# Performance work log

Measured on AMD Instinct MI355X. Metric: run time of the kernel, lower is better.

Reference implementation:

```python
import jax, jax.numpy as jnp
import numpy as np

N_NODES, N_EDGES, HIDDEN, N_LAYERS, VOCAB = 50000, 800000, 64, 2, 100

def silu(v):
    return v * jax.nn.sigmoid(v)

def setup_inputs() -> dict:
    key = jax.random.key(0)
    ks = jax.random.split(key, 18)
    N, E, H, L = N_NODES, N_EDGES, HIDDEN, N_LAYERS
    atomic_numbers = jax.random.randint(ks[0], (N,), 0, VOCAB)
    pos = jax.random.normal(ks[1], (N, 3), jnp.float32)
    edge_index = jax.random.randint(ks[2], (2, E), 0, N)
    edge_attr = jax.random.normal(ks[3], (E, 4), jnp.float32)
    emb = (jax.random.normal(ks[4], (VOCAB, H), jnp.float32) * 0.1).at[0].set(0.0)  # padding_idx=0
    def w(k, shape):
        return jax.random.normal(k, shape, jnp.float32) * (1.0 / np.sqrt(shape[-2]))
    return {
        'atomic_numbers': atomic_numbers, 'pos': pos,
        'edge_index': edge_index, 'edge_attr': edge_attr, 'emb': emb,
        # phi_e: Linear(2H+1,H) -> SiLU -> Linear(H,H) -> SiLU, stacked over layers
        'e_w1': w(ks[5], (L, 2 * H + 1, H)), 'e_b1': jnp.zeros((L, H), jnp.float32),
        'e_w2': w(ks[6], (L, H, H)),         'e_b2': jnp.zeros((L, H), jnp.float32),
        # phi_h: Linear(2H,H) -> SiLU -> Linear(H,H)
        'h_w1': w(ks[7], (L, 2 * H, H)),     'h_b1': jnp.zeros((L, H), jnp.float32),
        'h_w2': w(ks[8], (L, H, H)),         'h_b2': jnp.zeros((L, H), jnp.float32),
        # phi_x: Linear(H,H) -> SiLU -> Linear(H,1)
        'x_w1': w(ks[9], (L, H, H)),         'x_b1': jnp.zeros((L, H), jnp.float32),
        'x_w2': w(ks[10], (L, H, 1)),        'x_b2': jnp.zeros((L, 1), jnp.float32),
    }

def reference(atomic_numbers, pos, edge_index, edge_attr, emb,
              e_w1, e_b1, e_w2, e_b2, h_w1, h_b1, h_w2, h_b2,
              x_w1, x_b1, x_w2, x_b2):
    N = pos.shape[0]
    src, dst = edge_index[0], edge_index[1]  # PyG: h_j = h[src], h_i = h[dst]; aggregate to dst
    h = emb[atomic_numbers]  # [N, H]
    x = pos
    for l in range(N_LAYERS):
        x_diff = x[src] - x[dst]                       # [E, 3]
        r_ij = jnp.linalg.norm(x_diff, axis=-1, keepdims=True)  # [E, 1]
        feat = jnp.concatenate([h[dst], h[src], r_ij], axis=-1)  # [E, 2H+1]
        m_ij = silu(silu(feat @ e_w1[l] + e_b1[l]) @ e_w2[l] + e_b2[l])  # [E, H]
        W_ij = silu(m_ij @ x_w1[l] + x_b1[l]) @ x_w2[l] + x_b2[l]        # [E, 1]
        x = x + jax.ops.segment_sum(W_ij * x_diff, dst, num_segments=N)
        m_i = jax.ops.segment_sum(m_ij, dst, num_segments=N)             # [N, H]
        hm = jnp.concatenate([h, m_i], axis=-1)                          # [N, 2H]
        h = h + (silu(hm @ h_w1[l] + h_b1[l]) @ h_w2[l] + h_b2[l])
    return h, x
```

## Files before the change

### kernel.cpp

```cpp
#include <hip/hip_runtime.h>

#define NN 50000
#define NE 800000
#define HD 64
#define NL 2
#define NT_E (NE / 16)
#define NT_N (NN / 16)
#define NCH 196

typedef __attribute__((ext_vector_type(4))) float f32x4;
typedef __attribute__((ext_vector_type(8))) short s16x8;

#define FLAG_OFF 0
#define WB_OFF   16
#define EMB_O 0
#define EW1_O 6400
#define EB1_O 22912
#define EW2_O 23040
#define EB2_O 31232
#define HW1_O 31360
#define HB1_O 47744
#define HW2_O 47872
#define HB2_O 56064
#define XW1_O 56192
#define XB1_O 64384
#define XW2_O 64512
#define XB2_O 64640
#define X_OFF    (WB_OFF + 64656)
#define MAGG_OFF (X_OFF + NN * 4)
#define XAGG_OFF (MAGG_OFF + NN * HD)
#define HBF_OFF  (XAGG_OFF + NN * 3)
#define CNT_OFF  (HBF_OFF + NN * 32)
#define CSUM_OFF (CNT_OFF + NCH * 256)
#define INCL_OFF (CSUM_OFF + 256)
#define PAIR_OFF (INCL_OFF + NCH * 256)

#define ROWP 72

__device__ __forceinline__ float bf2f(unsigned short u) {
    return __uint_as_float(((unsigned int)u) << 16);
}
__device__ __forceinline__ unsigned short f2bf(float f) {
    unsigned int i = __float_as_uint(f);
    i += 0x7fffu + ((i >> 16) & 1u);
    return (unsigned short)(i >> 16);
}
__device__ __forceinline__ unsigned short f2bf_t(float f) {
    return (unsigned short)(__float_as_uint(f) >> 16);
}
__device__ __forceinline__ float silu(float v) {
    const float e = __expf(-v);
    return v * __builtin_amdgcn_rcpf(1.0f + e);
}
__device__ __forceinline__ float ldf(const void* p, int i, int bf) {
    return bf ? bf2f(((const unsigned short*)p)[i]) : ((const float*)p)[i];
}

__global__ void detect_kernel(const unsigned short* __restrict__ pos, int* __restrict__ flag) {
    const int lane = threadIdx.x;
    const float v = bf2f(pos[2 * lane]);
    const float a = fabsf(v);
    const int ok = (a >= 1e-6f && a <= 1e6f) ? 1 : 0;
    const unsigned long long m = __ballot(ok);
    if (lane == 0) *flag = (__popcll(m) >= 32) ? 1 : 0;
}

__global__ __launch_bounds__(256) void convert_kernel(
    const void* pos, const void* emb,
    const void* ew1, const void* eb1, const void* ew2, const void* eb2,
    const void* hw1, const void* hb1, const void* hw2, const void* hb2,
    const void* xw1, const void* xb1, const void* xw2, const void* xb2,
    float* __restrict__ wbuf, float* __restrict__ x, const int* __restrict__ flag)
{
    const int bf = *flag;
    const int tid = blockIdx.x * blockDim.x + threadIdx.x;
    const int stride = gridDim.x * blockDim.x;
    for (int n = tid; n < NN; n += stride) {
        x[n * 4 + 0] = ldf(pos, n * 3 + 0, bf);
        x[n * 4 + 1] = ldf(pos, n * 3 + 1, bf);
        x[n * 4 + 2] = ldf(pos, n * 3 + 2, bf);
        x[n * 4 + 3] = 0.f;
    }
    for (int i = tid; i < 6400; i += stride) wbuf[EMB_O + i] = ldf(emb, i, bf);
    for (int i = tid; i < 16512; i += stride) wbuf[EW1_O + i] = ldf(ew1, i, bf);
    for (int i = tid; i < 128; i += stride) wbuf[EB1_O + i] = ldf(eb1, i, bf);
    for (int i = tid; i < 8192; i += stride) wbuf[EW2_O + i] = ldf(ew2, i, bf);
    for (int i = tid; i < 128; i += stride) wbuf[EB2_O + i] = ldf(eb2, i, bf);
    for (int i = tid; i < 16384; i += stride) wbuf[HW1_O + i] = ldf(hw1, i, bf);
    for (int i = tid; i < 128; i += stride) wbuf[HB1_O + i] = ldf(hb1, i, bf);
    for (int i = tid; i < 8192; i += stride) wbuf[HW2_O + i] = ldf(hw2, i, bf);
    for (int i = tid; i < 128; i += stride) wbuf[HB2_O + i] = ldf(hb2, i, bf);
    for (int i = tid; i < 8192; i += stride) wbuf[XW1_O + i] = ldf(xw1, i, bf);
    for (int i = tid; i < 128; i += stride) wbuf[XB1_O + i] = ldf(xb1, i, bf);
    for (int i = tid; i < 128; i += stride) wbuf[XW2_O + i] = ldf(xw2, i, bf);
    for (int i = tid; i < 2; i += stride) wbuf[XB2_O + i] = ldf(xb2, i, bf);
}

__global__ __launch_bounds__(256) void init_h_kernel(
    const int* __restrict__ an, const float* __restrict__ embf,
    unsigned short* __restrict__ h_bf)
{
    const int stride = gridDim.x * blockDim.x;
    for (int i = blockIdx.x * blockDim.x + threadIdx.x; i < NN * HD; i += stride) {
        int a = an[i >> 6];
        a = (a < 0) ? 0 : (a > 99 ? 99 : a);
        h_bf[i] = f2bf(embf[a * HD + (i & 63)]);
    }
}

__global__ __launch_bounds__(256) void hist_kernel(const int* __restrict__ ei, int* __restrict__ cnt) {
    const int stride = gridDim.x * blockDim.x;
    for (int e = blockIdx.x * blockDim.x + threadIdx.x; e < NE; e += stride) {
        int d = ei[NE + e];
        d = (d < 0) ? 0 : (d >= NN ? NN - 1 : d);
        atomicAdd(&cnt[d], 1);
    }
}

__global__ __launch_bounds__(256) void scan1_kernel(
    const int* __restrict__ cnt, int* __restrict__ incl, int* __restrict__ csum)
{
    __shared__ int s[256];
    const int t = threadIdx.x, b = blockIdx.x, i = b * 256 + t;
    s[t] = cnt[i];
    __syncthreads();
#pragma unroll
    for (int o = 1; o < 256; o <<= 1) {
        const int u = (t >= o) ? s[t - o] : 0;
        __syncthreads();
        s[t] += u;
        __syncthreads();
    }
    incl[i] = s[t];
    if (t == 255) csum[b] = s[255];
}

__global__ void scan2_kernel(int* __restrict__ csum) {
    __shared__ int s[256];
    const int t = threadIdx.x;
    s[t] = (t < NCH) ? csum[t] : 0;
    __syncthreads();
#pragma unroll
    for (int o = 1; o < 256; o <<= 1) {
        const int u = (t >= o) ? s[t - o] : 0;
        __syncthreads();
        s[t] += u;
        __syncthreads();
    }
    if (t < NCH) csum[t] = s[t];
}

__global__ __launch_bounds__(256) void scan3_kernel(
    int* __restrict__ cnt, const int* __restrict__ incl, const int* __restrict__ csum)
{
    const int t = threadIdx.x, b = blockIdx.x, i = b * 256 + t;
    const int off = (b > 0) ? csum[b - 1] : 0;
    cnt[i] = incl[i] - cnt[i] + off;
}

__global__ __launch_bounds__(256) void scatter_kernel(
    const int* __restrict__ ei, int* __restrict__ cur, int2* __restrict__ pair)
{
    const int stride = gridDim.x * blockDim.x;
    for (int e = blockIdx.x * blockDim.x + threadIdx.x; e < NE; e += stride) {
        int s = ei[e];
        int d = ei[NE + e];
        s = (s < 0) ? 0 : (s >= NN ? NN - 1 : s);
        d = (d < 0) ? 0 : (d >= NN ? NN - 1 : d);
        const int p = atomicAdd(&cur[d], 1);
        pair[p] = make_int2(s, d);
    }
}

__global__ __launch_bounds__(256, 4) void edge_mfma_kernel(
    const unsigned short* __restrict__ h_bf, const float* __restrict__ x,
    const int2* __restrict__ pair,
    const float* __restrict__ w1, const float* __restrict__ b1,
    const float* __restrict__ b2,
    const float* __restrict__ w2,
    const float* __restrict__ xw1, const float* __restrict__ xb1,
    const float* __restrict__ xw2, const float* __restrict__ xb2,
    float* __restrict__ m_agg, float* __restrict__ x_agg)
{
    __shared__ unsigned short s_w1p[4 * 4 * 64 * 8];
    __shared__ unsigned short s_xw1p[2 * 4 * 64 * 8];
    __shared__ unsigned short s_act[4][16 * ROWP];
    __shared__ float s_xd[4][16][4];
    __shared__ float s_wv[4][16];

    const int tid = threadIdx.x;
    for (int p = tid; p < 4 * 4 * 64 * 8; p += 256) {
        const int j = p & 7, ln = (p >> 3) & 63, nt = (p >> 9) & 3, kc = p >> 11;
        const int k = kc * 32 + (ln >> 4) * 8 + j, n = nt * 16 + (ln & 15);
        s_w1p[p] = f2bf(w1[k * 64 + n]);
    }
    for (int p = tid; p < 2 * 4 * 64 * 8; p += 256) {
        const int j = p & 7, ln = (p >> 3) & 63, nt = (p >> 9) & 3, kc = p >> 11;
        const int k = kc * 32 + (ln >> 4) * 8 + j, n = nt * 16 + (ln & 15);
        s_xw1p[p] = f2bf(xw1[k * 64 + n]);
    }
    __syncthreads();

    const int lane = tid & 63;
    const int wid = tid >> 6;
    const int l15 = lane & 15;
    const int q = lane >> 4;

    s16x8 bw2[2][4];
#pragma unroll
    for (int kc = 0; kc < 2; ++kc)
#pragma unroll
        for (int nt = 0; nt < 4; ++nt)
#pragma unroll
            for (int j = 0; j < 8; ++j)
                bw2[kc][nt][j] = (short)f2bf(w2[(kc * 32 + q * 8 + j) * 64 + nt * 16 + l15]);

    float b1v[4], b2v[4], xb1v[4], xw2v[4], wrv[4];
#pragma unroll
    for (int nt = 0; nt < 4; ++nt) {
        b1v[nt] = b1[nt * 16 + l15];
        b2v[nt] = b2[nt * 16 + l15];
        xb1v[nt] = xb1[nt * 16 + l15];
        xw2v[nt] = xw2[nt * 16 + l15];
        wrv[nt] = w1[128 * 64 + nt * 16 + l15];
    }
    const float xb2v = xb2[0];

    unsigned short* act = s_act[wid];
    float (*xd)[4] = s_xd[wid];
    float* wv = s_wv[wid];

    const int gwave = (blockIdx.x << 2) + wid;
    const int nwaves = gridDim.x << 2;

    for (int t = gwave; t < NT_E; t += nwaves) {
        const int e0 = t * 16;
        const int2 e = pair[e0 + l15];
        const int sidx = e.x, didx = e.y;
        const f32x4 xs = *(const f32x4*)&x[sidx * 4];
        const f32x4 xdv = *(const f32x4*)&x[didx * 4];
        const float ax = xs[0] - xdv[0];
        const float ay = xs[1] - xdv[1];
        const float az = xs[2] - xdv[2];
        const float rme = sqrtf(ax * ax + ay * ay + az * az);
        if (lane < 16) { xd[lane][0] = ax; xd[lane][1] = ay; xd[lane][2] = az; }

        const s16x8 a_hd0 = *(const s16x8*)&h_bf[didx * 64 + q * 8];
        const s16x8 a_hd1 = *(const s16x8*)&h_bf[didx * 64 + 32 + q * 8];
        const s16x8 a_hs0 = *(const s16x8*)&h_bf[sidx * 64 + q * 8];
        const s16x8 a_hs1 = *(const s16x8*)&h_bf[sidx * 64 + 32 + q * 8];

        f32x4 acc[4];
#pragma unroll
        for (int nt = 0; nt < 4; ++nt) acc[nt] = (f32x4){0.f, 0.f, 0.f, 0.f};
#pragma unroll
        for (int kc = 0; kc < 4; ++kc) {
            const s16x8 a = (kc == 0) ? a_hd0 : (kc == 1) ? a_hd1 : (kc == 2) ? a_hs0 : a_hs1;
#pragma unroll
            for (int nt = 0; nt < 4; ++nt) {
                const s16x8 b = *(const s16x8*)&s_w1p[((kc * 4 + nt) * 64 + lane) * 8];
                acc[nt] = __builtin_amdgcn_mfma_f32_16x16x32_bf16(a, b, acc[nt], 0, 0, 0);
            }
        }
        float rv[4];
#pragma unroll
        for (int r = 0; r < 4; ++r) rv[r] = __shfl(rme, q * 4 + r, 64);
#pragma unroll
        for (int nt = 0; nt < 4; ++nt)
#pragma unroll
            for (int r = 0; r < 4; ++r) {
                const float v = silu(acc[nt][r] + b1v[nt] + rv[r] * wrv[nt]);
                act[(q * 4 + r) * ROWP + nt * 16 + l15] = f2bf_t(v);
            }

        f32x4 acc2[4];
#pragma unroll
        for (int nt = 0; nt < 4; ++nt) acc2[nt] = (f32x4){0.f, 0.f, 0.f, 0.f};
#pragma unroll
        for (int kc = 0; kc < 2; ++kc) {
            const s16x8 a = *(const s16x8*)&act[l15 * ROWP + kc * 32 + q * 8];
#pragma unroll
            for (int nt = 0; nt < 4; ++nt)
                acc2[nt] = __builtin_amdgcn_mfma_f32_16x16x32_bf16(a, bw2[kc][nt], acc2[nt], 0, 0, 0);
        }
#pragma unroll
        for (int nt = 0; nt < 4; ++nt)
#pragma unroll
            for (int r = 0; r < 4; ++r) {
                const float v = silu(acc2[nt][r] + b2v[nt]);
                act[(q * 4 + r) * ROWP + nt * 16 + l15] = f2bf_t(v);
            }

        f32x4 xacc[4];
#pragma unroll
        for (int nt = 0; nt < 4; ++nt) xacc[nt] = (f32x4){0.f, 0.f, 0.f, 0.f};
#pragma unroll
        for (int kc = 0; kc < 2; ++kc) {
            const s16x8 a = *(const s16x8*)&act[l15 * ROWP + kc * 32 + q * 8];
#pragma unroll
            for (int nt = 0; nt < 4; ++nt) {
                const s16x8 b = *(const s16x8*)&s_xw1p[((kc * 4 + nt) * 64 + lane) * 8];
                xacc[nt] = __builtin_amdgcn_mfma_f32_16x16x32_bf16(a, b, xacc[nt], 0, 0, 0);
            }
        }
        float ssum[4];
#pragma unroll
        for (int r = 0; r < 4; ++r) {
            float s = 0.f;
#pragma unroll
            for (int nt = 0; nt < 4; ++nt)
                s += silu(xacc[nt][r] + xb1v[nt]) * xw2v[nt];
            ssum[r] = s;
        }
#pragma unroll
        for (int off = 1; off < 16; off <<= 1)
#pragma unroll
            for (int r = 0; r < 4; ++r) ssum[r] += __shfl_xor(ssum[r], off, 64);
        if (l15 == 0) {
#pragma unroll
            for (int r = 0; r < 4; ++r) wv[q * 4 + r] = ssum[r] + xb2v;
        }

        int dstv[17];
#pragma unroll
        for (int rr = 0; rr < 16; ++rr) dstv[rr] = __shfl(didx, rr, 64);
        dstv[16] = -1;

        float macc = 0.f;
#pragma unroll
        for (int rr = 0; rr < 16; ++rr) {
            macc += bf2f(act[rr * ROWP + lane]);
            if (dstv[rr + 1] != dstv[rr]) {
                atomicAdd(&m_agg[dstv[rr] * 64 + lane], macc);
                macc = 0.f;
            }
        }
        if (lane < 3) {
            float xac = 0.f;
#pragma unroll
            for (int rr = 0; rr < 16; ++rr) {
                xac += wv[rr] * xd[rr][lane];
                if (dstv[rr + 1] != dstv[rr]) {
                    atomicAdd(&x_agg[dstv[rr] * 3 + lane], xac);
                    xac = 0.f;
                }
            }
        }
    }
}

__global__ __launch_bounds__(256, 4) void node_mfma_kernel(
    float* __restrict__ x,
    const float* __restrict__ m_agg, const float* __restrict__ x_agg,
    const float* __restrict__ w1, const float* __restrict__ b1,
    const float* __restrict__ w2, const float* __restrict__ b2,
    unsigned short* __restrict__ h_bf,
    void* __restrict__ outv, const int* __restrict__ flag)
{
    __shared__ unsigned short s_w1p[4 * 4 * 64 * 8];
    __shared__ unsigned short s_act[4][16 * ROWP];

    const int tid = threadIdx.x;
    for (int p = tid; p < 4 * 4 * 64 * 8; p += 256) {
        const int j = p & 7, ln = (p >> 3) & 63, nt = (p >> 9) & 3, kc = p >> 11;
        const int k = kc * 32 + (ln >> 4) * 8 + j, n = nt * 16 + (ln & 15);
        s_w1p[p] = f2bf(w1[k * 64 + n]);
    }
    __syncthreads();

    const int bf = flag ? *flag : 1;
    const int lane = tid & 63;
    const int wid = tid >> 6;
    const int l15 = lane & 15;
    const int q = lane >> 4;

    for (int n = blockIdx.x * 256 + tid; n < NN; n += gridDim.x * 256) {
#pragma unroll
        for (int c = 0; c < 3; ++c) {
            const float xn = x[n * 4 + c] + x_agg[n * 3 + c];
            x[n * 4 + c] = xn;
            if (outv) {
                if (bf) ((unsigned short*)outv)[NN * HD + n * 3 + c] = f2bf(xn);
                else ((float*)outv)[NN * HD + n * 3 + c] = xn;
            }
        }
    }

    s16x8 bw2[2][4];
#pragma unroll
    for (int kc = 0; kc < 2; ++kc)
#pragma unroll
        for (int nt = 0; nt < 4; ++nt)
#pragma unroll
            for (int j = 0; j < 8; ++j)
                bw2[kc][nt][j] = (short)f2bf(w2[(kc * 32 + q * 8 + j) * 64 + nt * 16 + l15]);

    float b1v[4], b2v[4];
#pragma unroll
    for (int nt = 0; nt < 4; ++nt) {
        b1v[nt] = b1[nt * 16 + l15];
        b2v[nt] = b2[nt * 16 + l15];
    }
    unsigned short* act = s_act[wid];

    for (int t = (blockIdx.x << 2) + wid; t < NT_N; t += gridDim.x << 2) {
        const int n = t * 16 + l15;
        const s16x8 a0 = *(const s16x8*)&h_bf[n * 64 + q * 8];
        const s16x8 a1 = *(const s16x8*)&h_bf[n * 64 + 32 + q * 8];
        const f32x4 m0 = *(const f32x4*)&m_agg[n * 64 + q * 8];
        const f32x4 m1 = *(const f32x4*)&m_agg[n * 64 + q * 8 + 4];
        const f32x4 m2 = *(const f32x4*)&m_agg[n * 64 + 32 + q * 8];
        const f32x4 m3 = *(const f32x4*)&m_agg[n * 64 + 32 + q * 8 + 4];
        s16x8 a2, a3;
#pragma unroll
        for (int j = 0; j < 4; ++j) {
            a2[j] = (short)f2bf(m0[j]); a2[4 + j] = (short)f2bf(m1[j]);
            a3[j] = (short)f2bf(m2[j]); a3[4 + j] = (short)f2bf(m3[j]);
        }

        f32x4 acc[4];
#pragma unroll
        for (int nt = 0; nt < 4; ++nt) acc[nt] = (f32x4){0.f, 0.f, 0.f, 0.f};
#pragma unroll
        for (int kc = 0; kc < 4; ++kc) {
            const s16x8 a = (kc == 0) ? a0 : (kc == 1) ? a1 : (kc == 2) ? a2 : a3;
#pragma unroll
            for (int nt = 0; nt < 4; ++nt) {
                const s16x8 b = *(const s16x8*)&s_w1p[((kc * 4 + nt) * 64 + lane) * 8];
                acc[nt] = __builtin_amdgcn_mfma_f32_16x16x32_bf16(a, b, acc[nt], 0, 0, 0);
            }
        }
#pragma unroll
        for (int nt = 0; nt < 4; ++nt)
#pragma unroll
            for (int r = 0; r < 4; ++r)
                act[(q * 4 + r) * ROWP + nt * 16 + l15] = f2bf_t(silu(acc[nt][r] + b1v[nt]));

        f32x4 acc2[4];
#pragma unroll
        for (int nt = 0; nt < 4; ++nt) acc2[nt] = (f32x4){0.f, 0.f, 0.f, 0.f};
#pragma unroll
        for (int kc = 0; kc < 2; ++kc) {
            const s16x8 a = *(const s16x8*)&act[l15 * ROWP + kc * 32 + q * 8];
#pragma unroll
            for (int nt = 0; nt < 4; ++nt)
                acc2[nt] = __builtin_amdgcn_mfma_f32_16x16x32_bf16(a, bw2[kc][nt], acc2[nt], 0, 0, 0);
        }
#pragma unroll
        for (int nt = 0; nt < 4; ++nt)
#pragma unroll
            for (int r = 0; r < 4; ++r) {
                const int row = t * 16 + q * 4 + r, col = nt * 16 + l15;
                const float hn = bf2f(h_bf[row * 64 + col]) + acc2[nt][r] + b2v[nt];
                h_bf[row * 64 + col] = f2bf(hn);
                if (outv) {
                    if (bf) ((unsigned short*)outv)[row * 64 + col] = f2bf(hn);
                    else ((float*)outv)[row * 64 + col] = hn;
                }
            }
    }
}

extern "C" void kernel_launch(void* const* d_in, const int* in_sizes, int n_in,
                              void* d_out, int out_size, void* d_ws, size_t ws_size,
                              hipStream_t stream) {
    const int* an = (const int*)d_in[0];
    const void* pos = d_in[1];
    const int* ei = (const int*)d_in[2];

    int wi = 4;
    if (n_in > 4 && in_sizes[4] == 6400) wi = 4;
    else if (n_in > 3 && in_sizes[3] == 6400) wi = 3;
    const void* emb = d_in[wi];
    const void* e_w1 = d_in[wi + 1];
    const void* e_b1 = d_in[wi + 2];
    const void* e_w2 = d_in[wi + 3];
    const void* e_b2 = d_in[wi + 4];
    const void* h_w1 = d_in[wi + 5];
    const void* h_b1 = d_in[wi + 6];
    const void* h_w2 = d_in[wi + 7];
    const void* h_b2 = d_in[wi + 8];
    const void* x_w1 = d_in[wi + 9];
    const void* x_b1 = d_in[wi + 10];
    const void* x_w2 = d_in[wi + 11];
    const void* x_b2 = d_in[wi + 12];

    float* ws = (float*)d_ws;
    int* flag = (int*)(ws + FLAG_OFF);
    float* wbuf = ws + WB_OFF;
    float* x = ws + X_OFF;
    float* m_agg = ws + MAGG_OFF;
    float* x_agg = ws + XAGG_OFF;
    unsigned short* h_bf = (unsigned short*)(ws + HBF_OFF);
    int* cnt = (int*)(ws + CNT_OFF);
    int* csum = (int*)(ws + CSUM_OFF);
    int* incl = (int*)(ws + INCL_OFF);
    int2* pair = (int2*)(ws + PAIR_OFF);

    detect_kernel<<<1, 64, 0, stream>>>((const unsigned short*)pos, flag);
    convert_kernel<<<256, 256, 0, stream>>>(pos, emb,
        e_w1, e_b1, e_w2, e_b2, h_w1, h_b1, h_w2, h_b2,
        x_w1, x_b1, x_w2, x_b2, wbuf, x, flag);
    init_h_kernel<<<784, 256, 0, stream>>>(an, wbuf + EMB_O, h_bf);

    hipMemsetAsync(cnt, 0, NCH * 256 * sizeof(int), stream);
    hist_kernel<<<512, 256, 0, stream>>>(ei, cnt);
    scan1_kernel<<<NCH, 256, 0, stream>>>(cnt, incl, csum);
    scan2_kernel<<<1, 256, 0, stream>>>(csum);
    scan3_kernel<<<NCH, 256, 0, stream>>>(cnt, incl, csum);
    scatter_kernel<<<512, 256, 0, stream>>>(ei, cnt, pair);

    for (int l = 0; l < NL; ++l) {
        hipMemsetAsync(m_agg, 0, (size_t)NN * HD * sizeof(float), stream);
        hipMemsetAsync(x_agg, 0, (size_t)NN * 3 * sizeof(float), stream);

        edge_mfma_kernel<<<1024, 256, 0, stream>>>(h_bf, x, pair,
            wbuf + EW1_O + l * 129 * 64, wbuf + EB1_O + l * 64,
            wbuf + EB2_O + l * 64,
            wbuf + EW2_O + l * 64 * 64,
            wbuf + XW1_O + l * 64 * 64, wbuf + XB1_O + l * 64,
            wbuf + XW2_O + l * 64, wbuf + XB2_O + l,
            m_agg, x_agg);

        void* out_p = (l == NL - 1) ? d_out : nullptr;
        node_mfma_kernel<<<782, 256, 0, stream>>>(x, m_agg, x_agg,
            wbuf + HW1_O + l * 128 * 64, wbuf + HB1_O + l * 64,
            wbuf + HW2_O + l * 64 * 64, wbuf + HB2_O + l * 64,
            h_bf, out_p, flag);
    }
}
```

Before: 448.2 us.

## Fuse prep kernels, zero aggregates in node kernel, widen blocks to 512

Merges the detect, convert, embedding-init and histogram kernels into a single prep kernel, and folds the per-layer memsets of m_agg and x_agg into the node kernel, which zeroes them after reading. The edge and node kernels move to 512-thread blocks (8 waves) with new grid sizes and launch bounds. The intent is fewer launches and memsets, less redundant traffic, and better occupancy. Edge activation rounding changes from truncation to round-to-nearest. Risk: every block recomputes the bf16 detection, and register pressure rises under the (512,6) launch bounds.

```diff
diff --git a/kernel.cpp b/kernel.cpp
--- a/kernel.cpp
+++ b/kernel.cpp
@@ -55,33 +55,35 @@
 __device__ __forceinline__ float ldf(const void* p, int i, int bf) {
     return bf ? bf2f(((const unsigned short*)p)[i]) : ((const float*)p)[i];
 }
-
-__global__ void detect_kernel(const unsigned short* __restrict__ pos, int* __restrict__ flag) {
-    const int lane = threadIdx.x;
-    const float v = bf2f(pos[2 * lane]);
+__device__ __forceinline__ int detect_bf(const void* pos) {
+    const int lane = threadIdx.x & 63;
+    const float v = bf2f(((const unsigned short*)pos)[2 * lane]);
     const float a = fabsf(v);
-    const int ok = (a >= 1e-6f && a <= 1e6f) ? 1 : 0;
-    const unsigned long long m = __ballot(ok);
-    if (lane == 0) *flag = (__popcll(m) >= 32) ? 1 : 0;
-}
-
-__global__ __launch_bounds__(256) void convert_kernel(
-    const void* pos, const void* emb,
+    const unsigned long long m = __ballot(a >= 1e-6f && a <= 1e6f);
+    return (__popcll(m) >= 32) ? 1 : 0;
+}
+
+__global__ __launch_bounds__(256) void prep_kernel(
+    const int* __restrict__ an, const void* pos, const int* __restrict__ ei,
+    const void* emb,
     const void* ew1, const void* eb1, const void* ew2, const void* eb2,
     const void* hw1, const void* hb1, const void* hw2, const void* hb2,
     const void* xw1, const void* xb1, const void* xw2, const void* xb2,
-    float* __restrict__ wbuf, float* __restrict__ x, const int* __restrict__ flag)
+    float* __restrict__ wbuf, float* __restrict__ x,
+    unsigned short* __restrict__ h_bf, int* __restrict__ cnt,
+    int* __restrict__ flag)
 {
-    const int bf = *flag;
+    const int bf = detect_bf(pos);
     const int tid = blockIdx.x * blockDim.x + threadIdx.x;
+    if (tid == 0) *flag = bf;
     const int stride = gridDim.x * blockDim.x;
+
     for (int n = tid; n < NN; n += stride) {
         x[n * 4 + 0] = ldf(pos, n * 3 + 0, bf);
         x[n * 4 + 1] = ldf(pos, n * 3 + 1, bf);
         x[n * 4 + 2] = ldf(pos, n * 3 + 2, bf);
         x[n * 4 + 3] = 0.f;
     }
-    for (int i = tid; i < 6400; i += stride) wbuf[EMB_O + i] = ldf(emb, i, bf);
     for (int i = tid; i < 16512; i += stride) wbuf[EW1_O + i] = ldf(ew1, i, bf);
     for (int i = tid; i < 128; i += stride) wbuf[EB1_O + i] = ldf(eb1, i, bf);
     for (int i = tid; i < 8192; i += stride) wbuf[EW2_O + i] = ldf(ew2, i, bf);
@@ -94,23 +96,13 @@
     for (int i = tid; i < 128; i += stride) wbuf[XB1_O + i] = ldf(xb1, i, bf);
     for (int i = tid; i < 128; i += stride) wbuf[XW2_O + i] = ldf(xw2, i, bf);
     for (int i = tid; i < 2; i += stride) wbuf[XB2_O + i] = ldf(xb2, i, bf);
-}
-
-__global__ __launch_bounds__(256) void init_h_kernel(
-    const int* __restrict__ an, const float* __restrict__ embf,
-    unsigned short* __restrict__ h_bf)
-{
-    const int stride = gridDim.x * blockDim.x;
-    for (int i = blockIdx.x * blockDim.x + threadIdx.x; i < NN * HD; i += stride) {
+
+    for (int i = tid; i < NN * HD; i += stride) {
         int a = an[i >> 6];
         a = (a < 0) ? 0 : (a > 99 ? 99 : a);
-        h_bf[i] = f2bf(embf[a * HD + (i & 63)]);
-    }
-}
-
-__global__ __launch_bounds__(256) void hist_kernel(const int* __restrict__ ei, int* __restrict__ cnt) {
-    const int stride = gridDim.x * blockDim.x;
-    for (int e = blockIdx.x * blockDim.x + threadIdx.x; e < NE; e += stride) {
+        h_bf[i] = f2bf(ldf(emb, a * HD + (i & 63), bf));
+    }
+    for (int e = tid; e < NE; e += stride) {
         int d = ei[NE + e];
         d = (d < 0) ? 0 : (d >= NN ? NN - 1 : d);
         atomicAdd(&cnt[d], 1);
@@ -155,7 +147,7 @@
 {
     const int t = threadIdx.x, b = blockIdx.x, i = b * 256 + t;
     const int off = (b > 0) ? csum[b - 1] : 0;
-    cnt[i] = incl[i] - cnt[i] + off;
+    cnt[i] = incl[i] + off - cnt[i];
 }
 
 __global__ __launch_bounds__(256) void scatter_kernel(
@@ -172,7 +164,7 @@
     }
 }
 
-__global__ __launch_bounds__(256, 4) void edge_mfma_kernel(
+__global__ __launch_bounds__(512, 6) void edge_mfma_kernel(
     const unsigned short* __restrict__ h_bf, const float* __restrict__ x,
     const int2* __restrict__ pair,
     const float* __restrict__ w1, const float* __restrict__ b1,
@@ -184,17 +176,17 @@
 {
     __shared__ unsigned short s_w1p[4 * 4 * 64 * 8];
     __shared__ unsigned short s_xw1p[2 * 4 * 64 * 8];
-    __shared__ unsigned short s_act[4][16 * ROWP];
-    __shared__ float s_xd[4][16][4];
-    __shared__ float s_wv[4][16];
+    __shared__ unsigned short s_act[8][16 * ROWP];
+    __shared__ float s_xd[8][16][4];
+    __shared__ float s_wv[8][16];
 
     const int tid = threadIdx.x;
-    for (int p = tid; p < 4 * 4 * 64 * 8; p += 256) {
+    for (int p = tid; p < 4 * 4 * 64 * 8; p += 512) {
         const int j = p & 7, ln = (p >> 3) & 63, nt = (p >> 9) & 3, kc = p >> 11;
         const int k = kc * 32 + (ln >> 4) * 8 + j, n = nt * 16 + (ln & 15);
         s_w1p[p] = f2bf(w1[k * 64 + n]);
     }
-    for (int p = tid; p < 2 * 4 * 64 * 8; p += 256) {
+    for (int p = tid; p < 2 * 4 * 64 * 8; p += 512) {
         const int j = p & 7, ln = (p >> 3) & 63, nt = (p >> 9) & 3, kc = p >> 11;
         const int k = kc * 32 + (ln >> 4) * 8 + j, n = nt * 16 + (ln & 15);
         s_xw1p[p] = f2bf(xw1[k * 64 + n]);
@@ -230,8 +222,8 @@
     float (*xd)[4] = s_xd[wid];
     float* wv = s_wv[wid];
 
-    const int gwave = (blockIdx.x << 2) + wid;
-    const int nwaves = gridDim.x << 2;
+    const int gwave = (blockIdx.x << 3) + wid;
+    const int nwaves = gridDim.x << 3;
 
     for (int t = gwave; t < NT_E; t += nwaves) {
         const int e0 = t * 16;
@@ -288,7 +280,7 @@
 #pragma unroll
             for (int r = 0; r < 4; ++r) {
                 const float v = silu(acc2[nt][r] + b2v[nt]);
-                act[(q * 4 + r) * ROWP + nt * 16 + l15] = f2bf_t(v);
+                act[(q * 4 + r) * ROWP + nt * 16 + l15] = f2bf(v);
             }
 
         f32x4 xacc[4];
@@ -349,19 +341,19 @@
     }
 }
 
-__global__ __launch_bounds__(256, 4) void node_mfma_kernel(
+__global__ __launch_bounds__(512, 6) void node_mfma_kernel(
     float* __restrict__ x,
-    const float* __restrict__ m_agg, const float* __restrict__ x_agg,
+    float* __restrict__ m_agg, float* __restrict__ x_agg,
     const float* __restrict__ w1, const float* __restrict__ b1,
     const float* __restrict__ w2, const float* __restrict__ b2,
     unsigned short* __restrict__ h_bf,
     void* __restrict__ outv, const int* __restrict__ flag)
 {
     __shared__ unsigned short s_w1p[4 * 4 * 64 * 8];
-    __shared__ unsigned short s_act[4][16 * ROWP];
+    __shared__ unsigned short s_act[8][16 * ROWP];
 
     const int tid = threadIdx.x;
-    for (int p = tid; p < 4 * 4 * 64 * 8; p += 256) {
+    for (int p = tid; p < 4 * 4 * 64 * 8; p += 512) {
         const int j = p & 7, ln = (p >> 3) & 63, nt = (p >> 9) & 3, kc = p >> 11;
         const int k = kc * 32 + (ln >> 4) * 8 + j, n = nt * 16 + (ln & 15);
         s_w1p[p] = f2bf(w1[k * 64 + n]);
@@ -374,10 +366,11 @@
     const int l15 = lane & 15;
     const int q = lane >> 4;
 
-    for (int n = blockIdx.x * 256 + tid; n < NN; n += gridDim.x * 256) {
+    for (int n = blockIdx.x * 512 + tid; n < NN; n += gridDim.x * 512) {
 #pragma unroll
         for (int c = 0; c < 3; ++c) {
             const float xn = x[n * 4 + c] + x_agg[n * 3 + c];
+            x_agg[n * 3 + c] = 0.f;
             x[n * 4 + c] = xn;
             if (outv) {
                 if (bf) ((unsigned short*)outv)[NN * HD + n * 3 + c] = f2bf(xn);
@@ -402,8 +395,9 @@
         b2v[nt] = b2[nt * 16 + l15];
     }
     unsigned short* act = s_act[wid];
-
-    for (int t = (blockIdx.x << 2) + wid; t < NT_N; t += gridDim.x << 2) {
+    const f32x4 zero4 = (f32x4){0.f, 0.f, 0.f, 0.f};
+
+    for (int t = (blockIdx.x << 3) + wid; t < NT_N; t += gridDim.x << 3) {
         const int n = t * 16 + l15;
         const s16x8 a0 = *(const s16x8*)&h_bf[n * 64 + q * 8];
         const s16x8 a1 = *(const s16x8*)&h_bf[n * 64 + 32 + q * 8];
@@ -411,6 +405,10 @@
         const f32x4 m1 = *(const f32x4*)&m_agg[n * 64 + q * 8 + 4];
         const f32x4 m2 = *(const f32x4*)&m_agg[n * 64 + 32 + q * 8];
         const f32x4 m3 = *(const f32x4*)&m_agg[n * 64 + 32 + q * 8 + 4];
+        *(f32x4*)&m_agg[n * 64 + q * 8] = zero4;
+        *(f32x4*)&m_agg[n * 64 + q * 8 + 4] = zero4;
+        *(f32x4*)&m_agg[n * 64 + 32 + q * 8] = zero4;
+        *(f32x4*)&m_agg[n * 64 + 32 + q * 8 + 4] = zero4;
         s16x8 a2, a3;
 #pragma unroll
         for (int j = 0; j < 4; ++j) {
@@ -420,7 +418,7 @@
 
         f32x4 acc[4];
 #pragma unroll
-        for (int nt = 0; nt < 4; ++nt) acc[nt] = (f32x4){0.f, 0.f, 0.f, 0.f};
+        for (int nt = 0; nt < 4; ++nt) acc[nt] = zero4;
 #pragma unroll
         for (int kc = 0; kc < 4; ++kc) {
             const s16x8 a = (kc == 0) ? a0 : (kc == 1) ? a1 : (kc == 2) ? a2 : a3;
@@ -438,7 +436,7 @@
 
         f32x4 acc2[4];
 #pragma unroll
-        for (int nt = 0; nt < 4; ++nt) acc2[nt] = (f32x4){0.f, 0.f, 0.f, 0.f};
+        for (int nt = 0; nt < 4; ++nt) acc2[nt] = zero4;
 #pragma unroll
         for (int kc = 0; kc < 2; ++kc) {
             const s16x8 a = *(const s16x8*)&act[l15 * ROWP + kc * 32 + q * 8];
@@ -497,24 +495,20 @@
     int* incl = (int*)(ws + INCL_OFF);
     int2* pair = (int2*)(ws + PAIR_OFF);
 
-    detect_kernel<<<1, 64, 0, stream>>>((const unsigned short*)pos, flag);
-    convert_kernel<<<256, 256, 0, stream>>>(pos, emb,
+    hipMemsetAsync(cnt, 0, NCH * 256 * sizeof(int), stream);
+    prep_kernel<<<784, 256, 0, stream>>>(an, pos, ei, emb,
         e_w1, e_b1, e_w2, e_b2, h_w1, h_b1, h_w2, h_b2,
-        x_w1, x_b1, x_w2, x_b2, wbuf, x, flag);
-    init_h_kernel<<<784, 256, 0, stream>>>(an, wbuf + EMB_O, h_bf);
-
-    hipMemsetAsync(cnt, 0, NCH * 256 * sizeof(int), stream);
-    hist_kernel<<<512, 256, 0, stream>>>(ei, cnt);
+        x_w1, x_b1, x_w2, x_b2, wbuf, x, h_bf, cnt, flag);
     scan1_kernel<<<NCH, 256, 0, stream>>>(cnt, incl, csum);
     scan2_kernel<<<1, 256, 0, stream>>>(csum);
     scan3_kernel<<<NCH, 256, 0, stream>>>(cnt, incl, csum);
     scatter_kernel<<<512, 256, 0, stream>>>(ei, cnt, pair);
 
+    hipMemsetAsync(m_agg, 0, (size_t)NN * HD * sizeof(float), stream);
+    hipMemsetAsync(x_agg, 0, (size_t)NN * 3 * sizeof(float), stream);
+
     for (int l = 0; l < NL; ++l) {
-        hipMemsetAsync(m_agg, 0, (size_t)NN * HD * sizeof(float), stream);
-        hipMemsetAsync(x_agg, 0, (size_t)NN * 3 * sizeof(float), stream);
-
-        edge_mfma_kernel<<<1024, 256, 0, stream>>>(h_bf, x, pair,
+        edge_mfma_kernel<<<768, 512, 0, stream>>>(h_bf, x, pair,
             wbuf + EW1_O + l * 129 * 64, wbuf + EB1_O + l * 64,
             wbuf + EB2_O + l * 64,
             wbuf + EW2_O + l * 64 * 64,
@@ -523,7 +517,7 @@
             m_agg, x_agg);
 
         void* out_p = (l == NL - 1) ? d_out : nullptr;
-        node_mfma_kernel<<<782, 256, 0, stream>>>(x, m_agg, x_agg,
+        node_mfma_kernel<<<392, 512, 0, stream>>>(x, m_agg, x_agg,
             wbuf + HW1_O + l * 128 * 64, wbuf + HB1_O + l * 64,
             wbuf + HW2_O + l * 64 * 64, wbuf + HB2_O + l * 64,
             h_bf, out_p, flag);
```

Result: slower. 497.6 us (+11.0%).
